# Performance work log

Measured on AMD Instinct MI355X. Metric: run time of the kernel, lower is better.

## Reference

```python
import jax, jax.numpy as jnp
import numpy as np

SEQ_LEN, HORIZON = 12, 12
B, N, DIN, DOUT, U = 16, 512, 2, 1, 64
NEG = -1e9


def _gat(x, W, a, b, mask):
    # x: (B, N, F_in); W: (F_in, G); a: (2, G); mask: (N, N) bool
    h = jnp.einsum('bnf,fg->bng', x, W)            # (B, N, G)
    src = jnp.einsum('bng,g->bn', h, a[0])         # (B, N)
    dst = jnp.einsum('bng,g->bn', h, a[1])         # (B, N)
    e = jax.nn.leaky_relu(src[:, :, None] + dst[:, None, :], 0.2)  # (B, N, N)
    e = jnp.where(mask[None], e, NEG)
    alpha = jax.nn.softmax(e, axis=-1)
    return jnp.einsum('bij,bjg->big', alpha, h) + b


def _cell(x, h_prev, W_ru, a_ru, b_ru, W_c, a_c, b_c, mask):
    # graph-attention GRU cell: x (B,N,Din), h_prev (B,N,U)
    xh = jnp.concatenate([x, h_prev], axis=-1)
    ru = jax.nn.sigmoid(_gat(xh, W_ru, a_ru, b_ru, mask))   # (B,N,2U)
    r, u = jnp.split(ru, 2, axis=-1)
    xc = jnp.concatenate([x, r * h_prev], axis=-1)
    c = jnp.tanh(_gat(xc, W_c, a_c, b_c, mask))
    return u * h_prev + (1.0 - u) * c


def setup_inputs() -> dict:
    key = jax.random.key(0)
    ks = jax.random.split(key, 16)
    s = 0.05
    inp = {
        'inputs': jax.random.normal(ks[0], (SEQ_LEN, B, N * DIN), jnp.float32),
        'adj': jax.random.uniform(ks[1], (N, N), jnp.float32),
        # encoder GAGRU cell (input_dim = DIN)
        'enc_W_ru': jax.random.normal(ks[2], (DIN + U, 2 * U), jnp.float32) * s,
        'enc_a_ru': jax.random.normal(ks[3], (2, 2 * U), jnp.float32) * s,
        'enc_b_ru': jnp.zeros((2 * U,), jnp.float32),
        'enc_W_c': jax.random.normal(ks[4], (DIN + U, U), jnp.float32) * s,
        'enc_a_c': jax.random.normal(ks[5], (2, U), jnp.float32) * s,
        'enc_b_c': jnp.zeros((U,), jnp.float32),
        # decoder GAGRU cell (input_dim = DOUT)
        'dec_W_ru': jax.random.normal(ks[6], (DOUT + U, 2 * U), jnp.float32) * s,
        'dec_a_ru': jax.random.normal(ks[7], (2, 2 * U), jnp.float32) * s,
        'dec_b_ru': jnp.zeros((2 * U,), jnp.float32),
        'dec_W_c': jax.random.normal(ks[8], (DOUT + U, U), jnp.float32) * s,
        'dec_a_c': jax.random.normal(ks[9], (2, U), jnp.float32) * s,
        'dec_b_c': jnp.zeros((U,), jnp.float32),
        # projection Linear(rnn_units -> output_dim)
        'proj_W': jax.random.normal(ks[10], (U, DOUT), jnp.float32) * s,
        'proj_b': jnp.zeros((DOUT,), jnp.float32),
    }
    return inp


def reference(inputs, adj, enc_W_ru, enc_a_ru, enc_b_ru, enc_W_c, enc_a_c, enc_b_c,
              dec_W_ru, dec_a_ru, dec_b_ru, dec_W_c, dec_a_c, dec_b_c, proj_W, proj_b):
    mask = (adj > 0.9) | jnp.eye(N, dtype=bool)
    x_seq = inputs.reshape(SEQ_LEN, B, N, DIN)

    # ---- encoder: scan GAGRU cell over seq_len ----
    def enc_step(h, x_t):
        h_new = _cell(x_t, h, enc_W_ru, enc_a_ru, enc_b_ru, enc_W_c, enc_a_c, enc_b_c, mask)
        return h_new, None

    h0 = jnp.zeros((B, N, U), inputs.dtype)
    h_enc, _ = jax.lax.scan(enc_step, h0, x_seq)

    def dec_step(carry, _):
        y_prev, h = carry
        h_new = _cell(y_prev, h, dec_W_ru, dec_a_ru, dec_b_ru, dec_W_c, dec_a_c, dec_b_c, mask)
        y = jnp.einsum('bnu,ud->bnd', h_new, proj_W) + proj_b  # (B, N, DOUT)
        return (y, h_new), y

    go = jnp.zeros((B, N, DOUT), inputs.dtype)
    _, outputs = jax.lax.scan(dec_step, (go, h_enc), None, length=HORIZON)
    return outputs  # (horizon, B, N, DOUT)
```

## Files before the change

kernel.cpp:

```cpp
#include <hip/hip_runtime.h>
#include <math.h>


#define NB 16
#define NN 512
#define NU 64
#define CAP 128
#define WPB 8

#define AS1 __attribute__((address_space(1)))
#define AS3 __attribute__((address_space(3)))

__device__ __forceinline__ void ld_lds16(float* lds_uniform, const float* g_perlane) {
#if __has_builtin(__builtin_amdgcn_global_load_lds)
  __builtin_amdgcn_global_load_lds((const AS1 unsigned int*)g_perlane,
                                   (AS3 unsigned int*)lds_uniform, 16, 0, 0);
#else
  int lane = threadIdx.x & 63;
  *(float4*)(lds_uniform + lane * 4) = *(const float4*)(g_perlane);
#endif
}

__device__ __forceinline__ void stage_weights(float* sW, const float* W, int TB,
                                              int w, int lane) {
  for (int c = w; c * 1024 < TB; c += WPB) {
    int off = c * 1024 + lane * 16;
    if (off < TB)
      ld_lds16((float*)((char*)sW + c * 1024), (const float*)((const char*)W + off));
  }
}

__device__ __forceinline__ float rlane(float v, int l) {
  return __int_as_float(__builtin_amdgcn_readlane(__float_as_int(v), l));
}
__device__ __forceinline__ int rlane_i(int v, int l) {
  return __builtin_amdgcn_readlane(v, l);
}
__device__ __forceinline__ float wave_max(float v) {
  #pragma unroll
  for (int s = 1; s < 64; s <<= 1) v = fmaxf(v, __shfl_xor(v, s));
  return v;
}
__device__ __forceinline__ float wave_sum(float v) {
  #pragma unroll
  for (int s = 1; s < 64; s <<= 1) v += __shfl_xor(v, s);
  return v;
}
__device__ __forceinline__ void wave_sum2(float& x, float& y) {
  #pragma unroll
  for (int s = 1; s < 64; s <<= 1) { x += __shfl_xor(x, s); y += __shfl_xor(y, s); }
}
__device__ __forceinline__ float fast_rcp(float x) {
#if __has_builtin(__builtin_amdgcn_rcpf)
  return __builtin_amdgcn_rcpf(x);
#else
  return 1.0f / x;
#endif
}
__device__ __forceinline__ float sigmoid_f(float x) {
  return fast_rcp(1.0f + __expf(-x));
}
__device__ __forceinline__ float tanh_f(float x) {
  return 1.0f - 2.0f * fast_rcp(__expf(2.0f * x) + 1.0f);
}

__global__ __launch_bounds__(64) void k_adj(const float* __restrict__ adj,
                                            int* __restrict__ cnt,
                                            int* __restrict__ idx) {
  int i = blockIdx.x;
  int l = threadIdx.x;
  int base = 0;
  #pragma unroll
  for (int c = 0; c < 8; ++c) {
    int j = c * 64 + l;
    bool pred = (adj[i * NN + j] > 0.9f) || (j == i);
    unsigned long long m = __ballot(pred);
    int pos = base + __popcll(m & ((1ull << l) - 1ull));
    if (pred && pos < CAP) idx[i * CAP + pos] = j;
    base += __popcll(m);
  }
  int total = base > CAP ? CAP : base;
  for (int p = total + l; p < CAP; p += 64) idx[i * CAP + p] = i;
  if (l == 0) cnt[i] = total;
}

template <int DIN>
__global__ __launch_bounds__(512, 6) void k_phaseB(
    const int* __restrict__ cnt, const int* __restrict__ idx,
    const float* __restrict__ h_ru, const float* __restrict__ src_ru,
    const float* __restrict__ dst_ru, const float* __restrict__ b_ru,
    const float* __restrict__ h, const float* __restrict__ x_ptr,
    const float* __restrict__ W_c, const float* __restrict__ a_c,
    float* __restrict__ h_c, float* __restrict__ src_c,
    float* __restrict__ dst_c, float* __restrict__ u_buf) {
  constexpr int TB = (DIN + NU) * NU * 4;
  __shared__ float sW[(DIN + NU) * NU];
  __shared__ float sh[WPB * NU];
  const int tid = threadIdx.x;
  const int w = tid >> 6, lane = tid & 63;

  stage_weights(sW, W_c, TB, w, lane);

  const int b = blockIdx.x >> 6;
  const int i = ((blockIdx.x & 63) << 3) | w;
  const int base_bi = (b << 9) + i;
  const float* __restrict__ hrb = h_ru + ((size_t)b << 16);
  const float* __restrict__ drb = dst_ru + (b << 9);

  const int c_ = cnt[i];
  const float si = src_ru[base_bi];
  const int j0 = idx[(i << 7) + lane];
  const int j1 = idx[(i << 7) + 64 + lane];
  float e0 = -1e30f, e1 = -1e30f;
  if (lane < c_)      { float t = si + drb[j0]; e0 = t >= 0.f ? t : 0.2f * t; }
  if (lane + 64 < c_) { float t = si + drb[j1]; e1 = t >= 0.f ? t : 0.2f * t; }
  float m = wave_max(fmaxf(e0, e1));
  float p0 = (lane < c_) ? __expf(e0 - m) : 0.f;
  float p1 = (lane + 64 < c_) ? __expf(e1 - m) : 0.f;
  float inv = fast_rcp(wave_sum(p0 + p1));
  p0 *= inv; p1 *= inv;

  const int g0 = lane << 1;
  float A0 = 0.f, A1 = 0.f, B0 = 0.f, B1 = 0.f;
  const int cc = (c_ + 15) & ~15;
  for (int base = 0; base < cc; base += 16) {
    float2 hv[16];
    #pragma unroll
    for (int q = 0; q < 16; ++q) {
      int jj = base + q;
      int sl = jj & 63;
      int j = (jj < 64) ? rlane_i(j0, sl) : rlane_i(j1, sl);
      hv[q] = *(const float2*)(hrb + (j << 7) + g0);
    }
    #pragma unroll
    for (int q = 0; q < 16; ++q) {
      int jj = base + q;
      int sl = jj & 63;
      float pv = (jj < 64) ? rlane(p0, sl) : rlane(p1, sl);
      if (q & 1) { B0 = fmaf(pv, hv[q].x, B0); B1 = fmaf(pv, hv[q].y, B1); }
      else       { A0 = fmaf(pv, hv[q].x, A0); A1 = fmaf(pv, hv[q].y, A1); }
    }
  }
  A0 += B0; A1 += B1;

  const float2 br = *(const float2*)(b_ru + g0);
  const float ru0 = sigmoid_f(A0 + br.x);
  const float ru1 = sigmoid_f(A1 + br.y);

  if (lane < 32) {
    float2 hh = *(const float2*)(h + ((size_t)base_bi << 6) + g0);
    *(float2*)&sh[(w << 6) + g0] = make_float2(ru0 * hh.x, ru1 * hh.y);
  } else {
    *(float2*)(u_buf + ((size_t)base_bi << 6) + (g0 - 64)) = make_float2(ru0, ru1);
  }

  __syncthreads();

  float acc;
  if (DIN == 2) {
    float2 xv = *(const float2*)(x_ptr + ((size_t)base_bi << 1));
    acc = xv.x * sW[lane];
    acc = fmaf(xv.y, sW[NU + lane], acc);
  } else {
    acc = x_ptr[base_bi] * sW[lane];
  }
  const float* __restrict__ sWh = sW + DIN * NU;
  const float* shw = sh + (w << 6);
  #pragma unroll
  for (int f2 = 0; f2 < 32; ++f2) {
    float2 rv = *(const float2*)(shw + 2 * f2);
    acc = fmaf(rv.x, sWh[(2 * f2) * NU + lane], acc);
    acc = fmaf(rv.y, sWh[(2 * f2 + 1) * NU + lane], acc);
  }
  h_c[((size_t)base_bi << 6) + lane] = acc;
  float s0 = acc * a_c[lane];
  float s1 = acc * a_c[NU + lane];
  wave_sum2(s0, s1);
  if (lane == 0) { src_c[base_bi] = s0; dst_c[base_bi] = s1; }
}

template <int UPD, int DIN_NEXT, int XMODE, int OUT>
__global__ __launch_bounds__(512, 6) void k_phaseA(
    const int* __restrict__ cnt, const int* __restrict__ idx,
    const float* __restrict__ h_c, const float* __restrict__ src_c,
    const float* __restrict__ dst_c, const float* __restrict__ b_c,
    const float* __restrict__ u_buf, float* __restrict__ h,
    const float* __restrict__ proj_W, const float* __restrict__ proj_b,
    float* __restrict__ out_slice, float* __restrict__ y_buf,
    const float* __restrict__ x_ptr,
    const float* __restrict__ W_ru, const float* __restrict__ a_ru,
    float* __restrict__ h_ru, float* __restrict__ src_ru,
    float* __restrict__ dst_ru) {
  constexpr int SWN = (DIN_NEXT > 0) ? (DIN_NEXT + NU) * 128 : 1;
  constexpr int TB = (DIN_NEXT > 0) ? SWN * 4 : 0;
  __shared__ float sW[SWN];
  __shared__ float sh[WPB * NU];
  const int tid = threadIdx.x;
  const int w = tid >> 6, lane = tid & 63;

  if (DIN_NEXT > 0) stage_weights(sW, W_ru, TB, w, lane);

  const int b = blockIdx.x >> 6;
  const int i = ((blockIdx.x & 63) << 3) | w;
  const int base_bi = (b << 9) + i;

  float hn = 0.f;
  if (UPD) {
    const float* __restrict__ hcb = h_c + ((size_t)b << 15);
    const float* __restrict__ dcb = dst_c + (b << 9);
    const int c_ = cnt[i];
    const float si = src_c[base_bi];
    const int j0 = idx[(i << 7) + lane];
    const int j1 = idx[(i << 7) + 64 + lane];
    float e0 = -1e30f, e1 = -1e30f;
    if (lane < c_)      { float t = si + dcb[j0]; e0 = t >= 0.f ? t : 0.2f * t; }
    if (lane + 64 < c_) { float t = si + dcb[j1]; e1 = t >= 0.f ? t : 0.2f * t; }
    float m = wave_max(fmaxf(e0, e1));
    float p0 = (lane < c_) ? __expf(e0 - m) : 0.f;
    float p1 = (lane + 64 < c_) ? __expf(e1 - m) : 0.f;
    float inv = fast_rcp(wave_sum(p0 + p1));
    p0 *= inv; p1 *= inv;

    float A = 0.f, Bacc = 0.f;
    const int cc = (c_ + 15) & ~15;
    for (int base = 0; base < cc; base += 16) {
      float hv[16];
      #pragma unroll
      for (int q = 0; q < 16; ++q) {
        int jj = base + q;
        int sl = jj & 63;
        int j = (jj < 64) ? rlane_i(j0, sl) : rlane_i(j1, sl);
        hv[q] = hcb[(j << 6) + lane];
      }
      #pragma unroll
      for (int q = 0; q < 16; ++q) {
        int jj = base + q;
        int sl = jj & 63;
        float pv = (jj < 64) ? rlane(p0, sl) : rlane(p1, sl);
        if (q & 1) Bacc = fmaf(pv, hv[q], Bacc);
        else       A = fmaf(pv, hv[q], A);
      }
    }
    A += Bacc;
    const float cc_ = tanh_f(A + b_c[lane]);
    const float u = u_buf[((size_t)base_bi << 6) + lane];
    const float ho = h[((size_t)base_bi << 6) + lane];
    hn = fmaf(u, ho - cc_, cc_);
  }
  h[((size_t)base_bi << 6) + lane] = hn;
  sh[(w << 6) + lane] = hn;

  float y = 0.f;
  if (OUT) {
    float t = wave_sum(hn * proj_W[lane]);
    y = t + proj_b[0];
    if (lane == 0) { out_slice[base_bi] = y; y_buf[base_bi] = y; }
  }

  if (DIN_NEXT > 0) {
    __syncthreads();
    const int g0 = lane << 1;
    float a0, a1;
    if (XMODE == 0) {
      if (DIN_NEXT == 2) {
        float2 xv = *(const float2*)(x_ptr + ((size_t)base_bi << 1));
        a0 = xv.x * sW[g0];
        a1 = xv.x * sW[g0 + 1];
        a0 = fmaf(xv.y, sW[128 + g0], a0);
        a1 = fmaf(xv.y, sW[128 + g0 + 1], a1);
      } else {
        float xv = x_ptr[base_bi];
        a0 = xv * sW[g0]; a1 = xv * sW[g0 + 1];
      }
    } else if (XMODE == 2) {
      a0 = y * sW[g0]; a1 = y * sW[g0 + 1];
    } else {
      a0 = 0.f; a1 = 0.f;
    }
    const float* __restrict__ sWh = sW + DIN_NEXT * 128;
    const float* shw = sh + (w << 6);
    #pragma unroll
    for (int f2 = 0; f2 < 32; ++f2) {
      float2 hp = *(const float2*)(shw + 2 * f2);
      float2 w0 = *(const float2*)(sWh + (2 * f2) * 128 + g0);
      float2 w1 = *(const float2*)(sWh + (2 * f2 + 1) * 128 + g0);
      a0 = fmaf(hp.x, w0.x, a0); a1 = fmaf(hp.x, w0.y, a1);
      a0 = fmaf(hp.y, w1.x, a0); a1 = fmaf(hp.y, w1.y, a1);
    }
    *(float2*)(h_ru + ((size_t)base_bi << 7) + g0) = make_float2(a0, a1);
    const float2 ar0 = *(const float2*)(a_ru + g0);
    const float2 ar1 = *(const float2*)(a_ru + 128 + g0);
    float s0 = a0 * ar0.x + a1 * ar0.y;
    float s1 = a0 * ar1.x + a1 * ar1.y;
    wave_sum2(s0, s1);
    if (lane == 0) { src_ru[base_bi] = s0; dst_ru[base_bi] = s1; }
  }
}

extern "C" void kernel_launch(void* const* d_in, const int* in_sizes, int n_in,
                              void* d_out, int out_size, void* d_ws, size_t ws_size,
                              hipStream_t stream) {
  (void)in_sizes; (void)n_in; (void)out_size; (void)ws_size;
  const float* inputs   = (const float*)d_in[0];
  const float* adj      = (const float*)d_in[1];
  const float* enc_W_ru = (const float*)d_in[2];
  const float* enc_a_ru = (const float*)d_in[3];
  const float* enc_b_ru = (const float*)d_in[4];
  const float* enc_W_c  = (const float*)d_in[5];
  const float* enc_a_c  = (const float*)d_in[6];
  const float* enc_b_c  = (const float*)d_in[7];
  const float* dec_W_ru = (const float*)d_in[8];
  const float* dec_a_ru = (const float*)d_in[9];
  const float* dec_b_ru = (const float*)d_in[10];
  const float* dec_W_c  = (const float*)d_in[11];
  const float* dec_a_c  = (const float*)d_in[12];
  const float* dec_b_c  = (const float*)d_in[13];
  const float* proj_W   = (const float*)d_in[14];
  const float* proj_b   = (const float*)d_in[15];
  float* out = (float*)d_out;

  char* ws = (char*)d_ws;
  int*   cnt    = (int*)ws;
  int*   idx    = (int*)(ws + 2048);
  float* h      = (float*)(ws + 264192);
  float* h_ru   = (float*)(ws + 2361344);
  float* src_ru = (float*)(ws + 6555648);
  float* dst_ru = (float*)(ws + 6588416);
  float* h_c    = (float*)(ws + 6621184);
  float* src_c  = (float*)(ws + 8718336);
  float* dst_c  = (float*)(ws + 8751104);
  float* u_buf  = (float*)(ws + 8783872);
  float* y_buf  = (float*)(ws + 10881024);

  hipMemsetAsync(y_buf, 0, NB * NN * sizeof(float), stream);
  k_adj<<<NN, 64, 0, stream>>>(adj, cnt, idx);

  const int GRID = (NB * NN) / WPB;

  k_phaseA<0, 2, 0, 0><<<GRID, 512, 0, stream>>>(cnt, idx, h_c, src_c, dst_c,
      enc_b_c, u_buf, h, proj_W, proj_b, nullptr, y_buf,
      inputs, enc_W_ru, enc_a_ru, h_ru, src_ru, dst_ru);

  for (int t = 0; t < 12; ++t) {
    k_phaseB<2><<<GRID, 512, 0, stream>>>(cnt, idx, h_ru, src_ru, dst_ru, enc_b_ru,
        h, inputs + (size_t)t * NB * NN * 2, enc_W_c, enc_a_c,
        h_c, src_c, dst_c, u_buf);
    if (t < 11)
      k_phaseA<1, 2, 0, 0><<<GRID, 512, 0, stream>>>(cnt, idx, h_c, src_c, dst_c,
          enc_b_c, u_buf, h, proj_W, proj_b, nullptr, y_buf,
          inputs + (size_t)(t + 1) * NB * NN * 2, enc_W_ru, enc_a_ru,
          h_ru, src_ru, dst_ru);
    else
      k_phaseA<1, 1, 1, 0><<<GRID, 512, 0, stream>>>(cnt, idx, h_c, src_c, dst_c,
          enc_b_c, u_buf, h, proj_W, proj_b, nullptr, y_buf,
          nullptr, dec_W_ru, dec_a_ru, h_ru, src_ru, dst_ru);
  }

  for (int k = 0; k < 12; ++k) {
    k_phaseB<1><<<GRID, 512, 0, stream>>>(cnt, idx, h_ru, src_ru, dst_ru, dec_b_ru,
        h, y_buf, dec_W_c, dec_a_c, h_c, src_c, dst_c, u_buf);
    if (k < 11)
      k_phaseA<1, 1, 2, 1><<<GRID, 512, 0, stream>>>(cnt, idx, h_c, src_c, dst_c,
          dec_b_c, u_buf, h, proj_W, proj_b, out + (size_t)k * NB * NN, y_buf,
          nullptr, dec_W_ru, dec_a_ru, h_ru, src_ru, dst_ru);
    else
      k_phaseA<1, 0, 1, 1><<<GRID, 512, 0, stream>>>(cnt, idx, h_c, src_c, dst_c,
          dec_b_c, u_buf, h, proj_W, proj_b, out + (size_t)k * NB * NN, y_buf,
          nullptr, dec_W_ru, dec_a_ru, h_ru, src_ru, dst_ru);
  }
}
```

Before: 905.3 us.

## Fuse all GRU cell phases into one persistent cooperative kernel with grid syncs

Replaces roughly 49 separate phase kernel launches with a single cooperative kernel of 256 blocks of 1024 threads. Each wave owns two (batch,node) rows for the whole sequence and keeps hidden state, u, y and src scores in registers, so the h, u_buf, y_buf and src buffers and the memset are gone. Weights are staged to LDS once per encoder and once per decoder, and the kernel uses grid.sync between phases. The trade-offs are grid-wide barrier cost, lower occupancy from a fixed grid, and heavier per-wave register and readlane use.

```diff
diff --git a/kernel.cpp b/kernel.cpp
--- a/kernel.cpp
+++ b/kernel.cpp
@@ -1,29 +1,32 @@
 #include <hip/hip_runtime.h>
+#include <hip/hip_cooperative_groups.h>
 #include <math.h>
+
+namespace cg = cooperative_groups;
 
 
 #define NB 16
 #define NN 512
 #define NU 64
 #define CAP 128
-#define WPB 8
+#define NBLK 256
+#define NWAVE 16
 
 #define AS1 __attribute__((address_space(1)))
 #define AS3 __attribute__((address_space(3)))
 
-__device__ __forceinline__ void ld_lds16(float* lds_uniform, const float* g_perlane) {
+__device__ __forceinline__ void ld_lds16(float* lds_u, const float* g) {
 #if __has_builtin(__builtin_amdgcn_global_load_lds)
-  __builtin_amdgcn_global_load_lds((const AS1 unsigned int*)g_perlane,
-                                   (AS3 unsigned int*)lds_uniform, 16, 0, 0);
+  __builtin_amdgcn_global_load_lds((const AS1 unsigned int*)g,
+                                   (AS3 unsigned int*)lds_u, 16, 0, 0);
 #else
   int lane = threadIdx.x & 63;
-  *(float4*)(lds_uniform + lane * 4) = *(const float4*)(g_perlane);
+  *(float4*)(lds_u + lane * 4) = *(const float4*)g;
 #endif
 }
-
 __device__ __forceinline__ void stage_weights(float* sW, const float* W, int TB,
                                               int w, int lane) {
-  for (int c = w; c * 1024 < TB; c += WPB) {
+  for (int c = w; c * 1024 < TB; c += NWAVE) {
     int off = c * 1024 + lane * 16;
     if (off < TB)
       ld_lds16((float*)((char*)sW + c * 1024), (const float*)((const char*)W + off));
@@ -84,216 +87,220 @@
   if (l == 0) cnt[i] = total;
 }
 
-template <int DIN>
-__global__ __launch_bounds__(512, 6) void k_phaseB(
+__global__ __launch_bounds__(1024, 4) void k_garnn(
+    const float* __restrict__ inputs,
     const int* __restrict__ cnt, const int* __restrict__ idx,
-    const float* __restrict__ h_ru, const float* __restrict__ src_ru,
-    const float* __restrict__ dst_ru, const float* __restrict__ b_ru,
-    const float* __restrict__ h, const float* __restrict__ x_ptr,
-    const float* __restrict__ W_c, const float* __restrict__ a_c,
-    float* __restrict__ h_c, float* __restrict__ src_c,
-    float* __restrict__ dst_c, float* __restrict__ u_buf) {
-  constexpr int TB = (DIN + NU) * NU * 4;
-  __shared__ float sW[(DIN + NU) * NU];
-  __shared__ float sh[WPB * NU];
-  const int tid = threadIdx.x;
-  const int w = tid >> 6, lane = tid & 63;
-
-  stage_weights(sW, W_c, TB, w, lane);
-
-  const int b = blockIdx.x >> 6;
-  const int i = ((blockIdx.x & 63) << 3) | w;
-  const int base_bi = (b << 9) + i;
-  const float* __restrict__ hrb = h_ru + ((size_t)b << 16);
-  const float* __restrict__ drb = dst_ru + (b << 9);
-
-  const int c_ = cnt[i];
-  const float si = src_ru[base_bi];
-  const int j0 = idx[(i << 7) + lane];
-  const int j1 = idx[(i << 7) + 64 + lane];
-  float e0 = -1e30f, e1 = -1e30f;
-  if (lane < c_)      { float t = si + drb[j0]; e0 = t >= 0.f ? t : 0.2f * t; }
-  if (lane + 64 < c_) { float t = si + drb[j1]; e1 = t >= 0.f ? t : 0.2f * t; }
-  float m = wave_max(fmaxf(e0, e1));
-  float p0 = (lane < c_) ? __expf(e0 - m) : 0.f;
-  float p1 = (lane + 64 < c_) ? __expf(e1 - m) : 0.f;
-  float inv = fast_rcp(wave_sum(p0 + p1));
-  p0 *= inv; p1 *= inv;
-
-  const int g0 = lane << 1;
-  float A0 = 0.f, A1 = 0.f, B0 = 0.f, B1 = 0.f;
-  const int cc = (c_ + 15) & ~15;
-  for (int base = 0; base < cc; base += 16) {
-    float2 hv[16];
-    #pragma unroll
-    for (int q = 0; q < 16; ++q) {
-      int jj = base + q;
-      int sl = jj & 63;
-      int j = (jj < 64) ? rlane_i(j0, sl) : rlane_i(j1, sl);
-      hv[q] = *(const float2*)(hrb + (j << 7) + g0);
-    }
-    #pragma unroll
-    for (int q = 0; q < 16; ++q) {
-      int jj = base + q;
-      int sl = jj & 63;
-      float pv = (jj < 64) ? rlane(p0, sl) : rlane(p1, sl);
-      if (q & 1) { B0 = fmaf(pv, hv[q].x, B0); B1 = fmaf(pv, hv[q].y, B1); }
-      else       { A0 = fmaf(pv, hv[q].x, A0); A1 = fmaf(pv, hv[q].y, A1); }
-    }
-  }
-  A0 += B0; A1 += B1;
-
-  const float2 br = *(const float2*)(b_ru + g0);
-  const float ru0 = sigmoid_f(A0 + br.x);
-  const float ru1 = sigmoid_f(A1 + br.y);
-
-  if (lane < 32) {
-    float2 hh = *(const float2*)(h + ((size_t)base_bi << 6) + g0);
-    *(float2*)&sh[(w << 6) + g0] = make_float2(ru0 * hh.x, ru1 * hh.y);
-  } else {
-    *(float2*)(u_buf + ((size_t)base_bi << 6) + (g0 - 64)) = make_float2(ru0, ru1);
-  }
-
+    const float* __restrict__ enc_W_ru, const float* __restrict__ enc_a_ru,
+    const float* __restrict__ enc_b_ru, const float* __restrict__ enc_W_c,
+    const float* __restrict__ enc_a_c, const float* __restrict__ enc_b_c,
+    const float* __restrict__ dec_W_ru, const float* __restrict__ dec_a_ru,
+    const float* __restrict__ dec_b_ru, const float* __restrict__ dec_W_c,
+    const float* __restrict__ dec_a_c, const float* __restrict__ dec_b_c,
+    const float* __restrict__ proj_W, const float* __restrict__ proj_b,
+    float* __restrict__ h_ru, float* __restrict__ dst_ru_g,
+    float* __restrict__ h_c, float* __restrict__ dst_c_g,
+    float* __restrict__ out) {
+  __shared__ float sWru[8448];
+  __shared__ float sWc[4224];
+  cg::grid_group grid = cg::this_grid();
+  const int tid = threadIdx.x, w = tid >> 6, lane = tid & 63;
+
+  stage_weights(sWru, enc_W_ru, 33792, w, lane);
+  stage_weights(sWc, enc_W_c, 16896, w, lane);
+
+  const int wave_gid = blockIdx.x * NWAVE + w;
+  int bi_[2], b_[2], c_[2], j0_[2], j1_[2];
+  float hn_[2] = {0.f, 0.f};
+  float src_ru_[2], src_c_[2], u_[2];
+  float y_[2] = {0.f, 0.f};
+  #pragma unroll
+  for (int n = 0; n < 2; ++n) {
+    int bi = 2 * wave_gid + n;
+    int i = bi & 511;
+    bi_[n] = bi; b_[n] = bi >> 9;
+    c_[n] = cnt[i];
+    j0_[n] = idx[(i << 7) + lane];
+    j1_[n] = idx[(i << 7) + 64 + lane];
+  }
   __syncthreads();
 
-  float acc;
-  if (DIN == 2) {
-    float2 xv = *(const float2*)(x_ptr + ((size_t)base_bi << 1));
-    acc = xv.x * sW[lane];
-    acc = fmaf(xv.y, sW[NU + lane], acc);
-  } else {
-    acc = x_ptr[base_bi] * sW[lane];
-  }
-  const float* __restrict__ sWh = sW + DIN * NU;
-  const float* shw = sh + (w << 6);
-  #pragma unroll
-  for (int f2 = 0; f2 < 32; ++f2) {
-    float2 rv = *(const float2*)(shw + 2 * f2);
-    acc = fmaf(rv.x, sWh[(2 * f2) * NU + lane], acc);
-    acc = fmaf(rv.y, sWh[(2 * f2 + 1) * NU + lane], acc);
-  }
-  h_c[((size_t)base_bi << 6) + lane] = acc;
-  float s0 = acc * a_c[lane];
-  float s1 = acc * a_c[NU + lane];
-  wave_sum2(s0, s1);
-  if (lane == 0) { src_c[base_bi] = s0; dst_c[base_bi] = s1; }
-}
-
-template <int UPD, int DIN_NEXT, int XMODE, int OUT>
-__global__ __launch_bounds__(512, 6) void k_phaseA(
-    const int* __restrict__ cnt, const int* __restrict__ idx,
-    const float* __restrict__ h_c, const float* __restrict__ src_c,
-    const float* __restrict__ dst_c, const float* __restrict__ b_c,
-    const float* __restrict__ u_buf, float* __restrict__ h,
-    const float* __restrict__ proj_W, const float* __restrict__ proj_b,
-    float* __restrict__ out_slice, float* __restrict__ y_buf,
-    const float* __restrict__ x_ptr,
-    const float* __restrict__ W_ru, const float* __restrict__ a_ru,
-    float* __restrict__ h_ru, float* __restrict__ src_ru,
-    float* __restrict__ dst_ru) {
-  constexpr int SWN = (DIN_NEXT > 0) ? (DIN_NEXT + NU) * 128 : 1;
-  constexpr int TB = (DIN_NEXT > 0) ? SWN * 4 : 0;
-  __shared__ float sW[SWN];
-  __shared__ float sh[WPB * NU];
-  const int tid = threadIdx.x;
-  const int w = tid >> 6, lane = tid & 63;
-
-  if (DIN_NEXT > 0) stage_weights(sW, W_ru, TB, w, lane);
-
-  const int b = blockIdx.x >> 6;
-  const int i = ((blockIdx.x & 63) << 3) | w;
-  const int base_bi = (b << 9) + i;
-
-  float hn = 0.f;
-  if (UPD) {
-    const float* __restrict__ hcb = h_c + ((size_t)b << 15);
-    const float* __restrict__ dcb = dst_c + (b << 9);
-    const int c_ = cnt[i];
-    const float si = src_c[base_bi];
-    const int j0 = idx[(i << 7) + lane];
-    const int j1 = idx[(i << 7) + 64 + lane];
-    float e0 = -1e30f, e1 = -1e30f;
-    if (lane < c_)      { float t = si + dcb[j0]; e0 = t >= 0.f ? t : 0.2f * t; }
-    if (lane + 64 < c_) { float t = si + dcb[j1]; e1 = t >= 0.f ? t : 0.2f * t; }
-    float m = wave_max(fmaxf(e0, e1));
-    float p0 = (lane < c_) ? __expf(e0 - m) : 0.f;
-    float p1 = (lane + 64 < c_) ? __expf(e1 - m) : 0.f;
-    float inv = fast_rcp(wave_sum(p0 + p1));
-    p0 *= inv; p1 *= inv;
-
-    float A = 0.f, Bacc = 0.f;
-    const int cc = (c_ + 15) & ~15;
-    for (int base = 0; base < cc; base += 16) {
-      float hv[16];
-      #pragma unroll
-      for (int q = 0; q < 16; ++q) {
-        int jj = base + q;
-        int sl = jj & 63;
-        int j = (jj < 64) ? rlane_i(j0, sl) : rlane_i(j1, sl);
-        hv[q] = hcb[(j << 6) + lane];
-      }
-      #pragma unroll
-      for (int q = 0; q < 16; ++q) {
-        int jj = base + q;
-        int sl = jj & 63;
-        float pv = (jj < 64) ? rlane(p0, sl) : rlane(p1, sl);
-        if (q & 1) Bacc = fmaf(pv, hv[q], Bacc);
-        else       A = fmaf(pv, hv[q], A);
-      }
-    }
-    A += Bacc;
-    const float cc_ = tanh_f(A + b_c[lane]);
-    const float u = u_buf[((size_t)base_bi << 6) + lane];
-    const float ho = h[((size_t)base_bi << 6) + lane];
-    hn = fmaf(u, ho - cc_, cc_);
-  }
-  h[((size_t)base_bi << 6) + lane] = hn;
-  sh[(w << 6) + lane] = hn;
-
-  float y = 0.f;
-  if (OUT) {
-    float t = wave_sum(hn * proj_W[lane]);
-    y = t + proj_b[0];
-    if (lane == 0) { out_slice[base_bi] = y; y_buf[base_bi] = y; }
-  }
-
-  if (DIN_NEXT > 0) {
-    __syncthreads();
+  #pragma unroll
+  for (int n = 0; n < 2; ++n) {
+    const float2 xv = *(const float2*)(inputs + (size_t)bi_[n] * 2);
     const int g0 = lane << 1;
-    float a0, a1;
-    if (XMODE == 0) {
-      if (DIN_NEXT == 2) {
-        float2 xv = *(const float2*)(x_ptr + ((size_t)base_bi << 1));
-        a0 = xv.x * sW[g0];
-        a1 = xv.x * sW[g0 + 1];
-        a0 = fmaf(xv.y, sW[128 + g0], a0);
-        a1 = fmaf(xv.y, sW[128 + g0 + 1], a1);
-      } else {
-        float xv = x_ptr[base_bi];
-        a0 = xv * sW[g0]; a1 = xv * sW[g0 + 1];
-      }
-    } else if (XMODE == 2) {
-      a0 = y * sW[g0]; a1 = y * sW[g0 + 1];
-    } else {
-      a0 = 0.f; a1 = 0.f;
-    }
-    const float* __restrict__ sWh = sW + DIN_NEXT * 128;
-    const float* shw = sh + (w << 6);
-    #pragma unroll
-    for (int f2 = 0; f2 < 32; ++f2) {
-      float2 hp = *(const float2*)(shw + 2 * f2);
-      float2 w0 = *(const float2*)(sWh + (2 * f2) * 128 + g0);
-      float2 w1 = *(const float2*)(sWh + (2 * f2 + 1) * 128 + g0);
-      a0 = fmaf(hp.x, w0.x, a0); a1 = fmaf(hp.x, w0.y, a1);
-      a0 = fmaf(hp.y, w1.x, a0); a1 = fmaf(hp.y, w1.y, a1);
-    }
-    *(float2*)(h_ru + ((size_t)base_bi << 7) + g0) = make_float2(a0, a1);
-    const float2 ar0 = *(const float2*)(a_ru + g0);
-    const float2 ar1 = *(const float2*)(a_ru + 128 + g0);
+    float a0 = xv.x * sWru[g0] + xv.y * sWru[128 + g0];
+    float a1 = xv.x * sWru[g0 + 1] + xv.y * sWru[128 + g0 + 1];
+    *(float2*)(h_ru + ((size_t)bi_[n] << 7) + g0) = make_float2(a0, a1);
+    const float2 ar0 = *(const float2*)(enc_a_ru + g0);
+    const float2 ar1 = *(const float2*)(enc_a_ru + 128 + g0);
     float s0 = a0 * ar0.x + a1 * ar0.y;
     float s1 = a0 * ar1.x + a1 * ar1.y;
     wave_sum2(s0, s1);
-    if (lane == 0) { src_ru[base_bi] = s0; dst_ru[base_bi] = s1; }
+    src_ru_[n] = s0;
+    if (lane == 0) dst_ru_g[bi_[n]] = s1;
+  }
+  grid.sync();
+
+  for (int cell = 0; cell < 24; ++cell) {
+    const bool enc = cell < 12;
+    const float* b_ru_p = enc ? enc_b_ru : dec_b_ru;
+    const float* a_c_p  = enc ? enc_a_c  : dec_a_c;
+    const float* b_c_p  = enc ? enc_b_c  : dec_b_c;
+
+    #pragma unroll
+    for (int n = 0; n < 2; ++n) {
+      const int b = b_[n], bi = bi_[n], cN = c_[n];
+      const float* __restrict__ hrb = h_ru + ((size_t)b << 16);
+      const float* __restrict__ drb = dst_ru_g + (b << 9);
+      const float si = src_ru_[n];
+      float x0, x1 = 0.f;
+      if (enc) {
+        float2 xv = *(const float2*)(inputs + (size_t)cell * 16384 + (size_t)bi * 2);
+        x0 = xv.x; x1 = xv.y;
+      } else {
+        x0 = y_[n];
+      }
+      float e0 = -1e30f, e1 = -1e30f;
+      if (lane < cN)      { float t = si + drb[j0_[n]]; e0 = t >= 0.f ? t : 0.2f * t; }
+      if (lane + 64 < cN) { float t = si + drb[j1_[n]]; e1 = t >= 0.f ? t : 0.2f * t; }
+      float m = wave_max(fmaxf(e0, e1));
+      float p0 = (lane < cN) ? __expf(e0 - m) : 0.f;
+      float p1 = (lane + 64 < cN) ? __expf(e1 - m) : 0.f;
+      float inv = fast_rcp(wave_sum(p0 + p1));
+      p0 *= inv; p1 *= inv;
+
+      const int g0 = lane << 1;
+      float A0 = 0.f, A1 = 0.f, B0 = 0.f, B1 = 0.f;
+      const int ccn = (cN + 15) & ~15;
+      for (int base = 0; base < ccn; base += 16) {
+        float2 hv[16];
+        #pragma unroll
+        for (int q = 0; q < 16; ++q) {
+          int jj = base + q; int sl = jj & 63;
+          int j = (jj < 64) ? rlane_i(j0_[n], sl) : rlane_i(j1_[n], sl);
+          hv[q] = *(const float2*)(hrb + (j << 7) + g0);
+        }
+        #pragma unroll
+        for (int q = 0; q < 16; ++q) {
+          int jj = base + q; int sl = jj & 63;
+          float pv = (jj < 64) ? rlane(p0, sl) : rlane(p1, sl);
+          if (q & 1) { B0 = fmaf(pv, hv[q].x, B0); B1 = fmaf(pv, hv[q].y, B1); }
+          else       { A0 = fmaf(pv, hv[q].x, A0); A1 = fmaf(pv, hv[q].y, A1); }
+        }
+      }
+      A0 += B0; A1 += B1;
+
+      const float2 br = *(const float2*)(b_ru_p + g0);
+      const float ru0 = sigmoid_f(A0 + br.x);
+      const float ru1 = sigmoid_f(A1 + br.y);
+      float rs0 = __shfl(ru0, lane >> 1), rs1 = __shfl(ru1, lane >> 1);
+      float r_l = (lane & 1) ? rs1 : rs0;
+      float us0 = __shfl(ru0, 32 + (lane >> 1)), us1 = __shfl(ru1, 32 + (lane >> 1));
+      u_[n] = (lane & 1) ? us1 : us0;
+      const float rh = r_l * hn_[n];
+
+      float acc = x0 * sWc[lane];
+      if (enc) acc = fmaf(x1, sWc[NU + lane], acc);
+      const float* __restrict__ sWh = sWc + (enc ? 2 : 1) * NU;
+      #pragma unroll
+      for (int f = 0; f < NU; ++f)
+        acc = fmaf(rlane(rh, f), sWh[f * NU + lane], acc);
+      h_c[((size_t)bi << 6) + lane] = acc;
+      float s0 = acc * a_c_p[lane];
+      float s1 = acc * a_c_p[NU + lane];
+      wave_sum2(s0, s1);
+      src_c_[n] = s0;
+      if (lane == 0) dst_c_g[bi] = s1;
+    }
+
+    if (cell == 11) {
+      __syncthreads();
+      stage_weights(sWru, dec_W_ru, 33280, w, lane);
+      stage_weights(sWc, dec_W_c, 16640, w, lane);
+      __syncthreads();
+    }
+    grid.sync();
+
+    const bool lastCell = (cell == 23);
+    const float* a_ru_p = (cell < 11) ? enc_a_ru : dec_a_ru;
+    #pragma unroll
+    for (int n = 0; n < 2; ++n) {
+      const int b = b_[n], bi = bi_[n], cN = c_[n];
+      const float* __restrict__ hcb = h_c + ((size_t)b << 15);
+      const float* __restrict__ dcb = dst_c_g + (b << 9);
+      const float si = src_c_[n];
+      float e0 = -1e30f, e1 = -1e30f;
+      if (lane < cN)      { float t = si + dcb[j0_[n]]; e0 = t >= 0.f ? t : 0.2f * t; }
+      if (lane + 64 < cN) { float t = si + dcb[j1_[n]]; e1 = t >= 0.f ? t : 0.2f * t; }
+      float m = wave_max(fmaxf(e0, e1));
+      float p0 = (lane < cN) ? __expf(e0 - m) : 0.f;
+      float p1 = (lane + 64 < cN) ? __expf(e1 - m) : 0.f;
+      float inv = fast_rcp(wave_sum(p0 + p1));
+      p0 *= inv; p1 *= inv;
+
+      float A = 0.f, Bc = 0.f;
+      const int ccn = (cN + 15) & ~15;
+      for (int base = 0; base < ccn; base += 16) {
+        float hv[16];
+        #pragma unroll
+        for (int q = 0; q < 16; ++q) {
+          int jj = base + q; int sl = jj & 63;
+          int j = (jj < 64) ? rlane_i(j0_[n], sl) : rlane_i(j1_[n], sl);
+          hv[q] = hcb[(j << 6) + lane];
+        }
+        #pragma unroll
+        for (int q = 0; q < 16; ++q) {
+          int jj = base + q; int sl = jj & 63;
+          float pv = (jj < 64) ? rlane(p0, sl) : rlane(p1, sl);
+          if (q & 1) Bc = fmaf(pv, hv[q], Bc);
+          else       A  = fmaf(pv, hv[q], A);
+        }
+      }
+      A += Bc;
+      const float ccv = tanh_f(A + b_c_p[lane]);
+      const float hn_new = fmaf(u_[n], hn_[n] - ccv, ccv);
+      hn_[n] = hn_new;
+
+      if (!enc) {
+        float t = wave_sum(hn_new * proj_W[lane]);
+        float yv = t + proj_b[0];
+        y_[n] = yv;
+        if (lane == 0) out[(size_t)(cell - 12) * (NB * NN) + bi] = yv;
+      }
+
+      if (!lastCell) {
+        const int g0 = lane << 1;
+        float x0n = 0.f, x1n = 0.f;
+        if (cell < 11) {
+          float2 xv = *(const float2*)(inputs + (size_t)(cell + 1) * 16384 + (size_t)bi * 2);
+          x0n = xv.x; x1n = xv.y;
+        } else if (cell >= 12) {
+          x0n = y_[n];
+        }
+        float a0 = x0n * sWru[g0], a1 = x0n * sWru[g0 + 1];
+        if (cell < 11) {
+          a0 = fmaf(x1n, sWru[128 + g0], a0);
+          a1 = fmaf(x1n, sWru[128 + g0 + 1], a1);
+        }
+        const float* __restrict__ sWh = sWru + ((cell < 11) ? 2 : 1) * 128;
+        #pragma unroll
+        for (int f = 0; f < NU; ++f) {
+          float hv = rlane(hn_new, f);
+          float2 wv = *(const float2*)(sWh + f * 128 + g0);
+          a0 = fmaf(hv, wv.x, a0);
+          a1 = fmaf(hv, wv.y, a1);
+        }
+        *(float2*)(h_ru + ((size_t)bi << 7) + g0) = make_float2(a0, a1);
+        const float2 ar0 = *(const float2*)(a_ru_p + g0);
+        const float2 ar1 = *(const float2*)(a_ru_p + 128 + g0);
+        float s0 = a0 * ar0.x + a1 * ar0.y;
+        float s1 = a0 * ar1.x + a1 * ar1.y;
+        wave_sum2(s0, s1);
+        src_ru_[n] = s0;
+        if (lane == 0) dst_ru_g[bi] = s1;
+      }
+    }
+    if (!lastCell) grid.sync();
   }
 }
 
@@ -322,50 +329,23 @@
   char* ws = (char*)d_ws;
   int*   cnt    = (int*)ws;
   int*   idx    = (int*)(ws + 2048);
-  float* h      = (float*)(ws + 264192);
-  float* h_ru   = (float*)(ws + 2361344);
-  float* src_ru = (float*)(ws + 6555648);
-  float* dst_ru = (float*)(ws + 6588416);
-  float* h_c    = (float*)(ws + 6621184);
-  float* src_c  = (float*)(ws + 8718336);
-  float* dst_c  = (float*)(ws + 8751104);
-  float* u_buf  = (float*)(ws + 8783872);
-  float* y_buf  = (float*)(ws + 10881024);
-
-  hipMemsetAsync(y_buf, 0, NB * NN * sizeof(float), stream);
+  float* h_ru   = (float*)(ws + 264192);
+  float* h_c    = (float*)(ws + 4458496);
+  float* dst_ru = (float*)(ws + 6555648);
+  float* dst_c  = (float*)(ws + 6588416);
+
   k_adj<<<NN, 64, 0, stream>>>(adj, cnt, idx);
 
-  const int GRID = (NB * NN) / WPB;
-
-  k_phaseA<0, 2, 0, 0><<<GRID, 512, 0, stream>>>(cnt, idx, h_c, src_c, dst_c,
-      enc_b_c, u_buf, h, proj_W, proj_b, nullptr, y_buf,
-      inputs, enc_W_ru, enc_a_ru, h_ru, src_ru, dst_ru);
-
-  for (int t = 0; t < 12; ++t) {
-    k_phaseB<2><<<GRID, 512, 0, stream>>>(cnt, idx, h_ru, src_ru, dst_ru, enc_b_ru,
-        h, inputs + (size_t)t * NB * NN * 2, enc_W_c, enc_a_c,
-        h_c, src_c, dst_c, u_buf);
-    if (t < 11)
-      k_phaseA<1, 2, 0, 0><<<GRID, 512, 0, stream>>>(cnt, idx, h_c, src_c, dst_c,
-          enc_b_c, u_buf, h, proj_W, proj_b, nullptr, y_buf,
-          inputs + (size_t)(t + 1) * NB * NN * 2, enc_W_ru, enc_a_ru,
-          h_ru, src_ru, dst_ru);
-    else
-      k_phaseA<1, 1, 1, 0><<<GRID, 512, 0, stream>>>(cnt, idx, h_c, src_c, dst_c,
-          enc_b_c, u_buf, h, proj_W, proj_b, nullptr, y_buf,
-          nullptr, dec_W_ru, dec_a_ru, h_ru, src_ru, dst_ru);
-  }
-
-  for (int k = 0; k < 12; ++k) {
-    k_phaseB<1><<<GRID, 512, 0, stream>>>(cnt, idx, h_ru, src_ru, dst_ru, dec_b_ru,
-        h, y_buf, dec_W_c, dec_a_c, h_c, src_c, dst_c, u_buf);
-    if (k < 11)
-      k_phaseA<1, 1, 2, 1><<<GRID, 512, 0, stream>>>(cnt, idx, h_c, src_c, dst_c,
-          dec_b_c, u_buf, h, proj_W, proj_b, out + (size_t)k * NB * NN, y_buf,
-          nullptr, dec_W_ru, dec_a_ru, h_ru, src_ru, dst_ru);
-    else
-      k_phaseA<1, 0, 1, 1><<<GRID, 512, 0, stream>>>(cnt, idx, h_c, src_c, dst_c,
-          dec_b_c, u_buf, h, proj_W, proj_b, out + (size_t)k * NB * NN, y_buf,
-          nullptr, dec_W_ru, dec_a_ru, h_ru, src_ru, dst_ru);
-  }
-}
+  void* args[] = {
+    (void*)&inputs, (void*)&cnt, (void*)&idx,
+    (void*)&enc_W_ru, (void*)&enc_a_ru, (void*)&enc_b_ru,
+    (void*)&enc_W_c,  (void*)&enc_a_c,  (void*)&enc_b_c,
+    (void*)&dec_W_ru, (void*)&dec_a_ru, (void*)&dec_b_ru,
+    (void*)&dec_W_c,  (void*)&dec_a_c,  (void*)&dec_b_c,
+    (void*)&proj_W, (void*)&proj_b,
+    (void*)&h_ru, (void*)&dst_ru, (void*)&h_c, (void*)&dst_c,
+    (void*)&out
+  };
+  hipLaunchCooperativeKernel((const void*)k_garnn, dim3(NBLK), dim3(1024),
+                             args, 0, stream);
+}
```

New measurement: 2.094 ms. 2.31x slower.

## Software-pipeline neighbor gathers with ping-pong buffers and raise occupancy bound

Applied to the files above, without the earlier changes.

The neighbor-aggregation loops in both phase kernels now split each 16-wide chunk into two 8-element register buffers. The next half-chunk's gathered rows are loaded while the current half is being accumulated, so memory latency overlaps with FMA work. The launch-bounds minimum-blocks hint also rises from 6 to 8, which forces the compiler to use fewer registers per thread to allow more resident waves. That risks spilling, especially with the extra live buffers.

```diff
diff --git a/kernel.cpp b/kernel.cpp
--- a/kernel.cpp
+++ b/kernel.cpp
@@ -85,7 +85,7 @@
 }
 
 template <int DIN>
-__global__ __launch_bounds__(512, 6) void k_phaseB(
+__global__ __launch_bounds__(512, 8) void k_phaseB(
     const int* __restrict__ cnt, const int* __restrict__ idx,
     const float* __restrict__ h_ru, const float* __restrict__ src_ru,
     const float* __restrict__ dst_ru, const float* __restrict__ b_ru,
@@ -122,23 +122,41 @@
 
   const int g0 = lane << 1;
   float A0 = 0.f, A1 = 0.f, B0 = 0.f, B1 = 0.f;
-  const int cc = (c_ + 15) & ~15;
-  for (int base = 0; base < cc; base += 16) {
-    float2 hv[16];
+  const int ccn = (c_ + 15) & ~15;
+  float2 va[8], vb[8];
+  #pragma unroll
+  for (int q = 0; q < 8; ++q) {
+    int j = rlane_i(j0, q);
+    va[q] = *(const float2*)(hrb + (j << 7) + g0);
+  }
+  for (int base = 0; base < ccn; base += 16) {
     #pragma unroll
-    for (int q = 0; q < 16; ++q) {
-      int jj = base + q;
-      int sl = jj & 63;
+    for (int q = 0; q < 8; ++q) {
+      int jj = base + 8 + q; int sl = jj & 63;
       int j = (jj < 64) ? rlane_i(j0, sl) : rlane_i(j1, sl);
-      hv[q] = *(const float2*)(hrb + (j << 7) + g0);
+      vb[q] = *(const float2*)(hrb + (j << 7) + g0);
     }
     #pragma unroll
-    for (int q = 0; q < 16; ++q) {
-      int jj = base + q;
-      int sl = jj & 63;
+    for (int q = 0; q < 8; ++q) {
+      int jj = base + q; int sl = jj & 63;
       float pv = (jj < 64) ? rlane(p0, sl) : rlane(p1, sl);
-      if (q & 1) { B0 = fmaf(pv, hv[q].x, B0); B1 = fmaf(pv, hv[q].y, B1); }
-      else       { A0 = fmaf(pv, hv[q].x, A0); A1 = fmaf(pv, hv[q].y, A1); }
+      if (q & 1) { B0 = fmaf(pv, va[q].x, B0); B1 = fmaf(pv, va[q].y, B1); }
+      else       { A0 = fmaf(pv, va[q].x, A0); A1 = fmaf(pv, va[q].y, A1); }
+    }
+    if (base + 16 < ccn) {
+      #pragma unroll
+      for (int q = 0; q < 8; ++q) {
+        int jj = base + 16 + q; int sl = jj & 63;
+        int j = (jj < 64) ? rlane_i(j0, sl) : rlane_i(j1, sl);
+        va[q] = *(const float2*)(hrb + (j << 7) + g0);
+      }
+    }
+    #pragma unroll
+    for (int q = 0; q < 8; ++q) {
+      int jj = base + 8 + q; int sl = jj & 63;
+      float pv = (jj < 64) ? rlane(p0, sl) : rlane(p1, sl);
+      if (q & 1) { B0 = fmaf(pv, vb[q].x, B0); B1 = fmaf(pv, vb[q].y, B1); }
+      else       { A0 = fmaf(pv, vb[q].x, A0); A1 = fmaf(pv, vb[q].y, A1); }
     }
   }
   A0 += B0; A1 += B1;
@@ -180,7 +198,7 @@
 }
 
 template <int UPD, int DIN_NEXT, int XMODE, int OUT>
-__global__ __launch_bounds__(512, 6) void k_phaseA(
+__global__ __launch_bounds__(512, 8) void k_phaseA(
     const int* __restrict__ cnt, const int* __restrict__ idx,
     const float* __restrict__ h_c, const float* __restrict__ src_c,
     const float* __restrict__ dst_c, const float* __restrict__ b_c,
@@ -222,23 +240,41 @@
     p0 *= inv; p1 *= inv;
 
     float A = 0.f, Bacc = 0.f;
-    const int cc = (c_ + 15) & ~15;
-    for (int base = 0; base < cc; base += 16) {
-      float hv[16];
+    const int ccn = (c_ + 15) & ~15;
+    float va[8], vb[8];
+    #pragma unroll
+    for (int q = 0; q < 8; ++q) {
+      int j = rlane_i(j0, q);
+      va[q] = hcb[(j << 6) + lane];
+    }
+    for (int base = 0; base < ccn; base += 16) {
       #pragma unroll
-      for (int q = 0; q < 16; ++q) {
-        int jj = base + q;
-        int sl = jj & 63;
+      for (int q = 0; q < 8; ++q) {
+        int jj = base + 8 + q; int sl = jj & 63;
         int j = (jj < 64) ? rlane_i(j0, sl) : rlane_i(j1, sl);
-        hv[q] = hcb[(j << 6) + lane];
+        vb[q] = hcb[(j << 6) + lane];
       }
       #pragma unroll
-      for (int q = 0; q < 16; ++q) {
-        int jj = base + q;
-        int sl = jj & 63;
+      for (int q = 0; q < 8; ++q) {
+        int jj = base + q; int sl = jj & 63;
         float pv = (jj < 64) ? rlane(p0, sl) : rlane(p1, sl);
-        if (q & 1) Bacc = fmaf(pv, hv[q], Bacc);
-        else       A = fmaf(pv, hv[q], A);
+        if (q & 1) Bacc = fmaf(pv, va[q], Bacc);
+        else       A = fmaf(pv, va[q], A);
+      }
+      if (base + 16 < ccn) {
+        #pragma unroll
+        for (int q = 0; q < 8; ++q) {
+          int jj = base + 16 + q; int sl = jj & 63;
+          int j = (jj < 64) ? rlane_i(j0, sl) : rlane_i(j1, sl);
+          va[q] = hcb[(j << 6) + lane];
+        }
+      }
+      #pragma unroll
+      for (int q = 0; q < 8; ++q) {
+        int jj = base + 8 + q; int sl = jj & 63;
+        float pv = (jj < 64) ? rlane(p0, sl) : rlane(p1, sl);
+        if (q & 1) Bacc = fmaf(pv, vb[q], Bacc);
+        else       A = fmaf(pv, vb[q], A);
       }
     }
     A += Bacc;
```

Measured after the change: 1.033 ms. 14.1% more time.
